# Kernel optimization log

Hardware: AMD Instinct MI355X
Metric: run time of the kernel (lower is better)

The kernel has to match this reference:

```python
import jax, jax.numpy as jnp
import numpy as np

# Module constants derived from init_kwargs
XYZ_MIN = np.array([-40.0, -40.0, -1.0], dtype=np.float32)
XYZ_MAX = np.array([40.0, 40.0, 5.4], dtype=np.float32)
STEPSIZE = 0.5
VOX = (200, 200, 16)
NUM_VOXELS = VOX[0] * VOX[1] * VOX[2]
VOXEL_SIZE = float((np.prod(XYZ_MAX - XYZ_MIN) / NUM_VOXELS) ** (1.0 / 3.0))  # = 0.4
N_SAMPLES = int(np.linalg.norm(np.array([VOX[0] // 2, VOX[1] // 2, VOX[2] // 2]) + 1) / STEPSIZE) + 1  # 287


def setup_inputs() -> dict:
    key = jax.random.key(0)
    k1, k2, k3 = jax.random.split(key, 3)
    rays_o = jax.random.uniform(k1, (6, 90, 160, 3), dtype=jnp.float32)   # camera origins near scene center
    rays_d = jax.random.normal(k2, (6, 90, 160, 3), dtype=jnp.float32)    # ray directions
    voxel = jax.random.normal(k3, (1, 200, 200, 16), dtype=jnp.float32)   # density grid (C=1, X, Y, Z)
    return {"rays_o": rays_o, "rays_d": rays_d, "voxel": voxel}


def trilinear_sample(grid, pts):
    """align_corners=True trilinear interpolation.
    grid: (C, Dx, Dy, Dz) laid out as (world-x, world-y, world-z) axes
    pts:  (M, 3) world coords. Out-of-range pts are clamped (they are masked later).
    Returns (C, M).
    """
    xyz_min = jnp.asarray(XYZ_MIN)
    xyz_max = jnp.asarray(XYZ_MAX)
    sizes = jnp.asarray(np.array(grid.shape[1:], dtype=np.float32))
    u = (pts - xyz_min) / (xyz_max - xyz_min)              # normalized [0,1]
    idx = jnp.clip(u * (sizes - 1.0), 0.0, sizes - 1.0)    # voxel-space coords
    i0 = jnp.clip(jnp.floor(idx), 0.0, sizes - 2.0).astype(jnp.int32)
    f = idx - i0.astype(idx.dtype)                          # fractional offsets
    x0, y0, z0 = i0[:, 0], i0[:, 1], i0[:, 2]
    fx, fy, fz = f[:, 0], f[:, 1], f[:, 2]
    out = jnp.zeros((grid.shape[0], pts.shape[0]), dtype=grid.dtype)
    for dx in (0, 1):
        wx = fx if dx else (1.0 - fx)
        for dy in (0, 1):
            wy = fy if dy else (1.0 - fy)
            for dz in (0, 1):
                wz = fz if dz else (1.0 - fz)
                corner = grid[:, x0 + dx, y0 + dy, z0 + dz]   # (C, M) gather
                out = out + corner * (wx * wy * wz)[None, :]
    return out


def reference(rays_o, rays_d, voxel):
    xyz_min = jnp.asarray(XYZ_MIN)
    xyz_max = jnp.asarray(XYZ_MAX)
    ro = rays_o.reshape(-1, 3)                                # (M, 3)
    rd = rays_d.reshape(-1, 3)                                # (M, 3)
    # eval-mode sampling: deterministic Zval shared by all rays
    zval = STEPSIZE * VOXEL_SIZE * jnp.arange(N_SAMPLES, dtype=jnp.float32)  # (N,)
    pts = ro[:, None, :] + rd[:, None, :] * zval[None, :, None]             # (M, N, 3)
    mask_out = jnp.any((pts < xyz_min) | (pts > xyz_max), axis=-1)          # (M, N)
    density = trilinear_sample(voxel, pts.reshape(-1, 3))                   # (1, M*N)
    density = density.reshape(pts.shape[0], N_SAMPLES)                      # (M, N)
    # alpha compositing (render_type='density')
    delta = zval[-1] - zval[-2]                                             # constant step length
    alpha = jnp.where(mask_out, 0.0, 1.0 - jnp.exp(-jax.nn.softplus(density) * delta))
    trans = jnp.cumprod(jnp.clip(1.0 - alpha, 1e-10, None), axis=-1)        # (M, N)
    alphainv_cum = jnp.concatenate([jnp.ones_like(trans[:, :1]), trans], axis=-1)
    weights = alpha * alphainv_cum[:, :-1]                                  # (M, N)
    depth = jnp.sum(weights * zval[None, :], axis=-1)                       # (M,)
    return depth
```

## Files before the change

kernel.cpp:

```cpp
#include <hip/hip_runtime.h>
#include <math.h>

#define N_RAYS 86400
#define N_SAMP 287
#define GRP_W  16
#define N_CHUNK 18
#define LOG2E 1.4426950408889634f

#define DPP(x, ctrl) __int_as_float(__builtin_amdgcn_update_dpp(             \
        0, __float_as_int(x), (ctrl), 0xF, 0xF, false))
#define ROW_SHR_OLD1(x, N) __int_as_float(__builtin_amdgcn_update_dpp(       \
        0x3f800000, __float_as_int(x), 0x110 | (N), 0xF, 0xF, false))
#define QPERM_X1 0xB1
#define QPERM_X2 0x4E
#define ROW_ROR4 0x124
#define ROW_ROR8 0x128

#define SWZ(x, pat) __int_as_float(__builtin_amdgcn_ds_swizzle(__float_as_int(x), (pat)))
#define SWZ_XOR(m)  (((m) << 10) | 0x1F)

__global__ __launch_bounds__(256) void nerf_depth_kernel(
    const float* __restrict__ rays_o,
    const float* __restrict__ rays_d,
    const float* __restrict__ voxel,
    float* __restrict__ depth_out,
    float stepf, float delta)
{
    const int lane = threadIdx.x & 63;
    const int sub  = lane & (GRP_W - 1);
    const int grp  = lane >> 4;
    const int wave = (blockIdx.x * blockDim.x + threadIdx.x) >> 6;
    const int ray  = wave * 4 + grp;

    const float ox = rays_o[3*ray+0], oy = rays_o[3*ray+1], oz = rays_o[3*ray+2];
    const float dx = rays_d[3*ray+0], dy = rays_d[3*ray+1], dz = rays_d[3*ray+2];

    const float cx1 = 199.0f / 80.0f;                  const float cx0 = 40.0f * cx1;
    const float cz1 = 15.0f / (5.4f - (-1.0f));        const float cz0 = 1.0f * cz1;
    const float negdelta = -delta;

    float T = 1.0f;
    float depth_acc = 0.0f;
    bool  done = false;

    for (int c = 0; c < N_CHUNK; ++c) {
        const int  s     = c * GRP_W + sub;
        const bool valid = (s < N_SAMP);
        const float z  = __fmul_rn(stepf, (float)s);
        const float px = __fadd_rn(ox, __fmul_rn(dx, z));
        const float py = __fadd_rn(oy, __fmul_rn(dy, z));
        const float pz = __fadd_rn(oz, __fmul_rn(dz, z));
        const bool inside = !((fmaxf(fabsf(px), fabsf(py)) > 40.0f) |
                              (pz < -1.0f) | (pz > 5.4f));
        const bool inb = (!done) && valid && inside;

        float g = 1.0f, az_negg = 0.0f;
        if (inb) {
            float ix = __builtin_fmaf(px, cx1, cx0);
            float iy = __builtin_fmaf(py, cx1, cx0);
            float iz = __builtin_fmaf(pz, cz1, cz0);
            int x0 = min((int)ix, 198);
            int y0 = min((int)iy, 198);
            int z0 = min((int)iz, 14);
            float fx = ix - (float)x0;
            float fy = iy - (float)y0;
            float fz = iz - (float)z0;
            const float* p00 = voxel + ((x0 * 200 + y0) * 16 + z0);
            float c000 = p00[0],    c001 = p00[1];
            float c010 = p00[16],   c011 = p00[17];
            float c100 = p00[3200], c101 = p00[3201];
            float c110 = p00[3216], c111 = p00[3217];
            float c00 = c000 + fz * (c001 - c000);
            float c01 = c010 + fz * (c011 - c010);
            float c10 = c100 + fz * (c101 - c100);
            float c11 = c110 + fz * (c111 - c110);
            float c0  = c00 + fy * (c01 - c00);
            float c1  = c10 + fy * (c11 - c10);
            float d   = c0  + fx * (c1  - c0);
            float e2 = exp2f(d * LOG2E);
            float lg = __log2f(1.0f + e2);
            g = exp2f(negdelta * lg);
            az_negg = (1.0f - g) * z;
        }

        float P = g;
        P *= ROW_SHR_OLD1(P, 1);
        P *= ROW_SHR_OLD1(P, 2);
        P *= ROW_SHR_OLD1(P, 4);
        P *= ROW_SHR_OLD1(P, 8);
        float E = ROW_SHR_OLD1(P, 1);

        depth_acc = __builtin_fmaf(az_negg, T * E, depth_acc);

        float rho = g;
        rho *= DPP(rho, QPERM_X1);
        rho *= DPP(rho, QPERM_X2);
        rho *= DPP(rho, ROW_ROR4);
        rho *= DPP(rho, ROW_ROR8);
        T *= rho;

        const unsigned long long bal = __ballot(inb);
        if (((unsigned)(bal >> (grp * GRP_W)) & 0xFFFFu) == 0u) done = true;
        if (T < 3e-4f) done = true;
        if (__all(done)) break;
    }

    depth_acc += SWZ(depth_acc, SWZ_XOR(1));
    depth_acc += SWZ(depth_acc, SWZ_XOR(2));
    depth_acc += SWZ(depth_acc, SWZ_XOR(4));
    depth_acc += SWZ(depth_acc, SWZ_XOR(8));
    if (sub == 0) depth_out[ray] = depth_acc;
}

extern "C" void kernel_launch(void* const* d_in, const int* in_sizes, int n_in,
                              void* d_out, int out_size, void* d_ws, size_t ws_size,
                              hipStream_t stream) {
    (void)in_sizes; (void)n_in; (void)d_ws; (void)ws_size; (void)out_size;
    const float* rays_o = (const float*)d_in[0];
    const float* rays_d = (const float*)d_in[1];
    const float* voxel  = (const float*)d_in[2];
    float* out = (float*)d_out;

    float rngz  = 5.4f - (-1.0f);
    float prod  = (80.0f * 80.0f) * rngz;
    float ratio = prod / 640000.0f;
    float stepf = (float)(0.5 * pow((double)ratio, 1.0 / 3.0));
    float delta = stepf * 286.0f - stepf * 285.0f;

    nerf_depth_kernel<<<N_RAYS / 16, 256, 0, stream>>>(rays_o, rays_d, voxel,
                                                       out, stepf, delta);
}
```

Baseline: 21.77 us.

## Use 32-lane ray groups with analytic ray-box exit chunk count

Each ray now gets 32 lanes instead of 16, so a wave handles two rays and processes samples in 9 chunks of 32. The exclusive prefix product is built with an inclusive scan plus a cross-row broadcast divided by g, and the row products are combined across halves with a swizzle. The per-chunk ballot used for early exit is replaced by a per-ray chunk count computed from a ray-box slab intersection. Voxel coordinates are now evaluated incrementally in index space. This doubles the block count and changes the work per lane. Dividing by g and evaluating voxel coordinates incrementally may shift floating-point results slightly.

```diff
diff --git a/kernel.cpp b/kernel.cpp
--- a/kernel.cpp
+++ b/kernel.cpp
@@ -3,14 +3,16 @@
 
 #define N_RAYS 86400
 #define N_SAMP 287
-#define GRP_W  16
-#define N_CHUNK 18
+#define GRP_W  32
+#define N_CHUNK 9
 #define LOG2E 1.4426950408889634f
 
 #define DPP(x, ctrl) __int_as_float(__builtin_amdgcn_update_dpp(             \
         0, __float_as_int(x), (ctrl), 0xF, 0xF, false))
 #define ROW_SHR_OLD1(x, N) __int_as_float(__builtin_amdgcn_update_dpp(       \
         0x3f800000, __float_as_int(x), 0x110 | (N), 0xF, 0xF, false))
+#define BCAST15_ROWS13(x) __int_as_float(__builtin_amdgcn_update_dpp(        \
+        0x3f800000, __float_as_int(x), 0x142, 0xA, 0xF, false))
 #define QPERM_X1 0xB1
 #define QPERM_X2 0x4E
 #define ROW_ROR4 0x124
@@ -28,40 +30,55 @@
 {
     const int lane = threadIdx.x & 63;
     const int sub  = lane & (GRP_W - 1);
-    const int grp  = lane >> 4;
+    const int half = lane >> 5;
     const int wave = (blockIdx.x * blockDim.x + threadIdx.x) >> 6;
-    const int ray  = wave * 4 + grp;
+    const int ray  = wave * 2 + half;
 
     const float ox = rays_o[3*ray+0], oy = rays_o[3*ray+1], oz = rays_o[3*ray+2];
     const float dx = rays_d[3*ray+0], dy = rays_d[3*ray+1], dz = rays_d[3*ray+2];
 
-    const float cx1 = 199.0f / 80.0f;                  const float cx0 = 40.0f * cx1;
-    const float cz1 = 15.0f / (5.4f - (-1.0f));        const float cz0 = 1.0f * cz1;
+    const float cx1 = 199.0f / 80.0f;              const float cx0 = 40.0f * cx1;
+    const float cz1 = 15.0f / (5.4f - (-1.0f));    const float cz0 = 1.0f * cz1;
     const float negdelta = -delta;
+
+    const float dix = __fmul_rn(dx, stepf) * cx1, oix = __builtin_fmaf(ox, cx1, cx0);
+    const float diy = __fmul_rn(dy, stepf) * cx1, oiy = __builtin_fmaf(oy, cx1, cx0);
+    const float diz = __fmul_rn(dz, stepf) * cz1, oiz = __builtin_fmaf(oz, cz1, cz0);
+
+    int nch;
+    {
+        float ivx = 1.0f / __fmul_rn(dx, stepf);
+        float ivy = 1.0f / __fmul_rn(dy, stepf);
+        float ivz = 1.0f / __fmul_rn(dz, stepf);
+        float tx = fmaxf((40.0f - ox) * ivx, (-40.0f - ox) * ivx);
+        float ty = fmaxf((40.0f - oy) * ivy, (-40.0f - oy) * ivy);
+        float tz = fmaxf((5.4f - oz) * ivz, (-1.0f - oz) * ivz);
+        float te = fminf(fminf(fminf(tx, ty), tz), 300.0f);
+        int s_stop = min((int)te + 2, N_SAMP);
+        nch = (s_stop + GRP_W - 1) >> 5;
+    }
 
     float T = 1.0f;
     float depth_acc = 0.0f;
-    bool  done = false;
 
     for (int c = 0; c < N_CHUNK; ++c) {
         const int  s     = c * GRP_W + sub;
-        const bool valid = (s < N_SAMP);
-        const float z  = __fmul_rn(stepf, (float)s);
+        const float sf   = (float)s;
+        const float z  = __fmul_rn(stepf, sf);
         const float px = __fadd_rn(ox, __fmul_rn(dx, z));
         const float py = __fadd_rn(oy, __fmul_rn(dy, z));
         const float pz = __fadd_rn(oz, __fmul_rn(dz, z));
-        const bool inside = !((fmaxf(fabsf(px), fabsf(py)) > 40.0f) |
-                              (pz < -1.0f) | (pz > 5.4f));
-        const bool inb = (!done) && valid && inside;
+        const bool inb = !((fmaxf(fabsf(px), fabsf(py)) > 40.0f) |
+                           (pz < -1.0f) | (pz > 5.4f)) && (s < N_SAMP);
 
-        float g = 1.0f, az_negg = 0.0f;
+        float g = 1.0f, az = 0.0f;
         if (inb) {
-            float ix = __builtin_fmaf(px, cx1, cx0);
-            float iy = __builtin_fmaf(py, cx1, cx0);
-            float iz = __builtin_fmaf(pz, cz1, cz0);
-            int x0 = min((int)ix, 198);
-            int y0 = min((int)iy, 198);
-            int z0 = min((int)iz, 14);
+            float ix = __builtin_fmaf(sf, dix, oix);
+            float iy = __builtin_fmaf(sf, diy, oiy);
+            float iz = __builtin_fmaf(sf, diz, oiz);
+            int x0 = min(max((int)ix, 0), 198);
+            int y0 = min(max((int)iy, 0), 198);
+            int z0 = min(max((int)iz, 0), 14);
             float fx = ix - (float)x0;
             float fy = iy - (float)y0;
             float fz = iz - (float)z0;
@@ -80,7 +97,7 @@
             float e2 = exp2f(d * LOG2E);
             float lg = __log2f(1.0f + e2);
             g = exp2f(negdelta * lg);
-            az_negg = (1.0f - g) * z;
+            az = (1.0f - g) * z;
         }
 
         float P = g;
@@ -88,27 +105,28 @@
         P *= ROW_SHR_OLD1(P, 2);
         P *= ROW_SHR_OLD1(P, 4);
         P *= ROW_SHR_OLD1(P, 8);
-        float E = ROW_SHR_OLD1(P, 1);
+        P *= BCAST15_ROWS13(P);
+        float E = P * __builtin_amdgcn_rcpf(g);
 
-        depth_acc = __builtin_fmaf(az_negg, T * E, depth_acc);
+        depth_acc = __builtin_fmaf(az, T * E, depth_acc);
 
         float rho = g;
         rho *= DPP(rho, QPERM_X1);
         rho *= DPP(rho, QPERM_X2);
         rho *= DPP(rho, ROW_ROR4);
         rho *= DPP(rho, ROW_ROR8);
+        rho *= SWZ(rho, SWZ_XOR(16));
         T *= rho;
 
-        const unsigned long long bal = __ballot(inb);
-        if (((unsigned)(bal >> (grp * GRP_W)) & 0xFFFFu) == 0u) done = true;
-        if (T < 3e-4f) done = true;
-        if (__all(done)) break;
+        const bool dead = (c + 1 >= nch) | (T < 3e-4f);
+        if (__all(dead)) break;
     }
 
     depth_acc += SWZ(depth_acc, SWZ_XOR(1));
     depth_acc += SWZ(depth_acc, SWZ_XOR(2));
     depth_acc += SWZ(depth_acc, SWZ_XOR(4));
     depth_acc += SWZ(depth_acc, SWZ_XOR(8));
+    depth_acc += SWZ(depth_acc, SWZ_XOR(16));
     if (sub == 0) depth_out[ray] = depth_acc;
 }
 
@@ -127,6 +145,6 @@
     float stepf = (float)(0.5 * pow((double)ratio, 1.0 / 3.0));
     float delta = stepf * 286.0f - stepf * 285.0f;
 
-    nerf_depth_kernel<<<N_RAYS / 16, 256, 0, stream>>>(rays_o, rays_d, voxel,
-                                                       out, stepf, delta);
+    nerf_depth_kernel<<<N_RAYS / 8, 256, 0, stream>>>(rays_o, rays_d, voxel,
+                                                      out, stepf, delta);
 }
```

After: 21.70 us. Within noise of the previous version (-0.3%).
